# Kernel optimization log

Measured on AMD Instinct MI355X. Metric: run time of the kernel, lower is better.

## Reference

```python
import jax, jax.numpy as jnp
import numpy as np
from math import sqrt

N = 8192
INPUT_SIZE = 256
D_MODEL = 256


def setup_inputs() -> dict:
    key = jax.random.key(0)
    k1, k2, k3, k4 = jax.random.split(key, 4)
    x = jax.random.normal(k1, (N, INPUT_SIZE), dtype=jnp.float32)
    adj = jax.random.randint(k2, (N, N), 0, 2, dtype=jnp.int32)
    # torch nn.Linear(input_size, d_model): weight [d_model, input_size], bias [d_model]
    bound = 1.0 / sqrt(INPUT_SIZE)
    Vw = jax.random.uniform(k3, (D_MODEL, INPUT_SIZE), dtype=jnp.float32, minval=-bound, maxval=bound)
    Vb = jax.random.uniform(k4, (D_MODEL,), dtype=jnp.float32, minval=-bound, maxval=bound)
    return {"x": x, "adj": adj, "Vw": Vw, "Vb": Vb}


def reference(x, adj, Vw, Vb):
    # value = V(x)
    value = x @ Vw.T + Vb                                  # [N, d_model]
    # scores = x x^T / sqrt(d_model), masked where adj == 0
    scores = (x @ x.T) * (1.0 / sqrt(D_MODEL))             # [N, N]
    scores = jnp.where(adj == 0, jnp.float32(-1e9), scores)
    p_attn = jax.nn.softmax(scores, axis=-1)               # [N, N]
    Vs = p_attn @ value                                    # [N, d_model]
    return (Vs, p_attn)
```

## Files before the change

### kernel.cpp

```cpp
#include <hip/hip_runtime.h>
#include <hip/hip_bf16.h>


#define NN 8192
#define DD 256

typedef __attribute__((ext_vector_type(8))) short bf16x8;
typedef __attribute__((ext_vector_type(4))) float f32x4;

__device__ __forceinline__ unsigned short f2bf(float f) {
  unsigned u = __builtin_bit_cast(unsigned, f);
  u += 0x7fffu + ((u >> 16) & 1u);
  return (unsigned short)(u >> 16);
}
__device__ __forceinline__ float bf2f(unsigned short h) {
  unsigned u = ((unsigned)h) << 16;
  return __builtin_bit_cast(float, u);
}
__device__ __forceinline__ unsigned pack2(float a, float b) {
  return (unsigned)f2bf(a) | ((unsigned)f2bf(b) << 16);
}

__global__ void k_prep_x(const float* __restrict__ x, unsigned short* __restrict__ xb) {
  int t = blockIdx.x * 256 + threadIdx.x;
  const float4* s = reinterpret_cast<const float4*>(x) + (size_t)t * 2;
  float4 f0 = s[0], f1 = s[1];
  uint4 o;
  o.x = pack2(f0.x, f0.y); o.y = pack2(f0.z, f0.w);
  o.z = pack2(f1.x, f1.y); o.w = pack2(f1.z, f1.w);
  reinterpret_cast<uint4*>(xb)[t] = o;
}

__global__ __launch_bounds__(256) void k_value(
    const float* __restrict__ Vw, const float* __restrict__ Vb,
    const unsigned short* __restrict__ xb, unsigned short* __restrict__ vT) {
  __shared__ unsigned short lB[64 * 256];
  int mb = blockIdx.x >> 2, nb = blockIdx.x & 3;
  int tid = threadIdx.x, lane = tid & 63, w = tid >> 6;
  int mw = w >> 1, nw = w & 1;
  {
    int n_l = tid >> 2, q = tid & 3;
#pragma unroll
    for (int o = 0; o < 8; ++o) {
      int k0 = q * 64 + o * 8;
      const float4* src = reinterpret_cast<const float4*>(Vw + (nb * 64 + n_l) * DD + k0);
      float4 g0 = src[0], g1 = src[1];
      uint4 pk;
      pk.x = pack2(g0.x, g0.y); pk.y = pack2(g0.z, g0.w);
      pk.z = pack2(g1.x, g1.y); pk.w = pack2(g1.z, g1.w);
      *reinterpret_cast<uint4*>(reinterpret_cast<char*>(lB) + n_l * 512 + ((k0 * 2) ^ ((n_l & 7) << 4))) = pk;
    }
  }
  bf16x8 aR[2][8];
#pragma unroll
  for (int mf = 0; mf < 2; ++mf) {
    int rg = mb * 64 + mw * 32 + mf * 16 + (lane & 15);
    const char* base = reinterpret_cast<const char*>(xb + (size_t)rg * DD);
#pragma unroll
    for (int ks = 0; ks < 8; ++ks)
      aR[mf][ks] = *reinterpret_cast<const bf16x8*>(base + ks * 64 + ((lane >> 4) * 16));
  }
  __syncthreads();
  f32x4 acc[2][2] = {};
#pragma unroll
  for (int ks = 0; ks < 8; ++ks) {
    int kb = ks * 64 + ((lane >> 4) * 16);
#pragma unroll
    for (int nf = 0; nf < 2; ++nf) {
      int n = nw * 32 + nf * 16 + (lane & 15);
      bf16x8 b = *reinterpret_cast<const bf16x8*>(reinterpret_cast<const char*>(lB) + n * 512 + (kb ^ ((n & 7) << 4)));
#pragma unroll
      for (int mf = 0; mf < 2; ++mf)
        acc[mf][nf] = __builtin_amdgcn_mfma_f32_16x16x32_bf16(aR[mf][ks], b, acc[mf][nf], 0, 0, 0);
    }
  }
#pragma unroll
  for (int nf = 0; nf < 2; ++nf) {
    int n_g = nb * 64 + nw * 32 + nf * 16 + (lane & 15);
    float vb = Vb[n_g];
#pragma unroll
    for (int mf = 0; mf < 2; ++mf) {
      int m_g = mb * 64 + mw * 32 + mf * 16 + ((lane >> 4) << 2);
      ushort4 h;
      h.x = f2bf(acc[mf][nf][0] + vb);
      h.y = f2bf(acc[mf][nf][1] + vb);
      h.z = f2bf(acc[mf][nf][2] + vb);
      h.w = f2bf(acc[mf][nf][3] + vb);
      *reinterpret_cast<ushort4*>(vT + (size_t)n_g * NN + m_g) = h;
    }
  }
}

__global__ __launch_bounds__(256) void k_pass1(
    const unsigned short* __restrict__ xb, const int* __restrict__ adj,
    unsigned short* __restrict__ ews, float* __restrict__ lpart) {
  __shared__ char smem[65536];
  int rb = blockIdx.x >> 6, cb = blockIdx.x & 63;
  int tid = threadIdx.x, lane = tid & 63, w = tid >> 6;
  int mw = w >> 1, wc = w & 1;
#pragma unroll
  for (int c = 0; c < 16; ++c) {
    int id = c * 256 + tid;
    int col = id >> 5, oct = id & 31;
    uint4 v = *reinterpret_cast<const uint4*>(xb + (size_t)(cb * 128 + col) * DD + oct * 8);
    *reinterpret_cast<uint4*>(smem + col * 512 + ((oct * 16) ^ ((col & 7) << 4))) = v;
  }
  bf16x8 aR[2][8];
#pragma unroll
  for (int mf = 0; mf < 2; ++mf) {
    int rg = rb * 64 + mw * 32 + mf * 16 + (lane & 15);
    const char* base = reinterpret_cast<const char*>(xb + (size_t)rg * DD);
#pragma unroll
    for (int ks = 0; ks < 8; ++ks)
      aR[mf][ks] = *reinterpret_cast<const bf16x8*>(base + ks * 64 + ((lane >> 4) * 16));
  }
  __syncthreads();
  int r0 = rb * 64 + mw * 32 + ((lane >> 4) << 2);
  int c0 = cb * 128 + wc * 64 + (lane & 15);
  int aj[2][4][4];
#pragma unroll
  for (int mf = 0; mf < 2; ++mf)
#pragma unroll
    for (int nf = 0; nf < 4; ++nf)
#pragma unroll
      for (int i = 0; i < 4; ++i)
        aj[mf][nf][i] = adj[(size_t)(r0 + mf * 16 + i) * NN + (c0 + nf * 16)];
  f32x4 acc[2][4] = {};
#pragma unroll
  for (int ks = 0; ks < 8; ++ks) {
    int kb = ks * 64 + ((lane >> 4) * 16);
#pragma unroll
    for (int nf = 0; nf < 4; ++nf) {
      int cc = wc * 64 + nf * 16 + (lane & 15);
      bf16x8 b = *reinterpret_cast<const bf16x8*>(smem + cc * 512 + (kb ^ ((cc & 7) << 4)));
#pragma unroll
      for (int mf = 0; mf < 2; ++mf)
        acc[mf][nf] = __builtin_amdgcn_mfma_f32_16x16x32_bf16(aR[mf][ks], b, acc[mf][nf], 0, 0, 0);
    }
  }
#pragma unroll
  for (int mf = 0; mf < 2; ++mf)
#pragma unroll
    for (int nf = 0; nf < 4; ++nf)
#pragma unroll
      for (int i = 0; i < 4; ++i) {
        float e = aj[mf][nf][i] ? __expf(acc[mf][nf][i] * 0.0625f) : 0.f;
        unsigned short h = f2bf(e);
        ews[(size_t)(r0 + mf * 16 + i) * NN + (c0 + nf * 16)] = h;
        acc[mf][nf][i] = bf2f(h);
      }
  __syncthreads();
  float* ls = reinterpret_cast<float*>(smem);
#pragma unroll
  for (int mf = 0; mf < 2; ++mf)
#pragma unroll
    for (int i = 0; i < 4; ++i) {
      float r = acc[mf][0][i] + acc[mf][1][i] + acc[mf][2][i] + acc[mf][3][i];
      r += __shfl_xor(r, 1); r += __shfl_xor(r, 2);
      r += __shfl_xor(r, 4); r += __shfl_xor(r, 8);
      if ((lane & 15) == 0)
        ls[wc * 64 + mw * 32 + mf * 16 + ((lane >> 4) << 2) + i] = r;
    }
  __syncthreads();
  if (tid < 64)
    lpart[(size_t)cb * NN + rb * 64 + tid] = ls[tid] + ls[64 + tid];
}

__global__ void k_reduce_l(const float* __restrict__ lpart, float* __restrict__ rl) {
  int i = blockIdx.x * 256 + threadIdx.x;
  float s = 0.f;
  for (int c = 0; c < 64; ++c) s += lpart[(size_t)c * NN + i];
  rl[i] = s > 0.f ? 1.f / s : 0.f;
}

__global__ __launch_bounds__(512) void k_pass2(
    const unsigned short* __restrict__ ews, const unsigned short* __restrict__ vT,
    const float* __restrict__ rl, float* __restrict__ pout, float* __restrict__ vsp) {
  __shared__ unsigned short lA[32 * 64];
  __shared__ unsigned short lB[256 * 64];
  int rb = blockIdx.x >> 1, ch = blockIdx.x & 1;
  int tid = threadIdx.x, lane = tid & 63, w = tid >> 6;
  int wr = w >> 2, wc = w & 3;
  int r0 = rb * 32, j0 = ch * 4096;
  int arow = tid >> 3, aoct = tid & 7;
  float rlA = 0.f;
  if (tid < 256) rlA = rl[r0 + arow];
  f32x4 acc[4] = {};
  for (int kt = 0; kt < 64; ++kt) {
    int jb = j0 + kt * 64;
    uint4 vA;
    if (tid < 256) vA = *reinterpret_cast<const uint4*>(ews + (size_t)(r0 + arow) * NN + jb + aoct * 8);
    uint4 vB[4];
#pragma unroll
    for (int q = 0; q < 4; ++q) {
      int id = q * 512 + tid, n = id >> 3, o = id & 7;
      vB[q] = *reinterpret_cast<const uint4*>(vT + (size_t)n * NN + jb + o * 8);
    }
    if (tid < 256) {
      const unsigned short* hh = reinterpret_cast<const unsigned short*>(&vA);
      float4 p0, p1;
      p0.x = bf2f(hh[0]) * rlA; p0.y = bf2f(hh[1]) * rlA;
      p0.z = bf2f(hh[2]) * rlA; p0.w = bf2f(hh[3]) * rlA;
      p1.x = bf2f(hh[4]) * rlA; p1.y = bf2f(hh[5]) * rlA;
      p1.z = bf2f(hh[6]) * rlA; p1.w = bf2f(hh[7]) * rlA;
      float4* pd = reinterpret_cast<float4*>(pout + (size_t)(r0 + arow) * NN + jb + aoct * 8);
      pd[0] = p0; pd[1] = p1;
      *reinterpret_cast<uint4*>(reinterpret_cast<char*>(lA) + arow * 128 + ((aoct * 16) ^ ((arow & 7) << 4))) = vA;
    }
#pragma unroll
    for (int q = 0; q < 4; ++q) {
      int id = q * 512 + tid, n = id >> 3, o = id & 7;
      *reinterpret_cast<uint4*>(reinterpret_cast<char*>(lB) + n * 128 + ((o * 16) ^ ((n & 7) << 4))) = vB[q];
    }
    __syncthreads();
#pragma unroll
    for (int ksp = 0; ksp < 2; ++ksp) {
      int kb = ksp * 64 + ((lane >> 4) * 16);
      int r = wr * 16 + (lane & 15);
      bf16x8 a = *reinterpret_cast<const bf16x8*>(reinterpret_cast<const char*>(lA) + r * 128 + (kb ^ ((r & 7) << 4)));
#pragma unroll
      for (int nf = 0; nf < 4; ++nf) {
        int n = wc * 64 + nf * 16 + (lane & 15);
        bf16x8 b = *reinterpret_cast<const bf16x8*>(reinterpret_cast<const char*>(lB) + n * 128 + (kb ^ ((n & 7) << 4)));
        acc[nf] = __builtin_amdgcn_mfma_f32_16x16x32_bf16(a, b, acc[nf], 0, 0, 0);
      }
    }
    __syncthreads();
  }
  float rli[4];
  int rbase = r0 + wr * 16 + ((lane >> 4) << 2);
#pragma unroll
  for (int i = 0; i < 4; ++i) rli[i] = rl[rbase + i];
#pragma unroll
  for (int nf = 0; nf < 4; ++nf) {
    int n = wc * 64 + nf * 16 + (lane & 15);
#pragma unroll
    for (int i = 0; i < 4; ++i)
      vsp[(size_t)(ch * NN + rbase + i) * DD + n] = acc[nf][i] * rli[i];
  }
}

__global__ void k_reduce_vs(const float* __restrict__ vsp, float* __restrict__ vout) {
  int t = blockIdx.x * 256 + threadIdx.x;
  float4 a = *reinterpret_cast<const float4*>(vsp + (size_t)t * 4);
  float4 b = *reinterpret_cast<const float4*>(vsp + (size_t)NN * DD + (size_t)t * 4);
  float4 r;
  r.x = a.x + b.x; r.y = a.y + b.y; r.z = a.z + b.z; r.w = a.w + b.w;
  *reinterpret_cast<float4*>(vout + (size_t)t * 4) = r;
}

extern "C" void kernel_launch(void* const* d_in, const int* in_sizes, int n_in,
                              void* d_out, int out_size, void* d_ws, size_t ws_size,
                              hipStream_t stream) {
  const float* x   = (const float*)d_in[0];
  const int*   adj = (const int*)d_in[1];
  const float* Vw  = (const float*)d_in[2];
  const float* Vb  = (const float*)d_in[3];
  float* out   = (float*)d_out;
  float* vs_out = out;
  float* p_out  = out + (size_t)NN * DD;
  char* ws = (char*)d_ws;
  unsigned short* xb  = (unsigned short*)(ws);
  unsigned short* vT  = (unsigned short*)(ws + ((size_t)4  << 20));
  float* lpart        = (float*)(ws + ((size_t)8  << 20));
  float* rl           = (float*)(ws + ((size_t)10 << 20));
  float* vsp          = (float*)(ws + ((size_t)11 << 20));
  unsigned short* ews = (unsigned short*)(ws + ((size_t)27 << 20));

  k_prep_x<<<dim3(1024), dim3(256), 0, stream>>>(x, xb);
  k_value<<<dim3(512), dim3(256), 0, stream>>>(Vw, Vb, xb, vT);
  k_pass1<<<dim3(8192), dim3(256), 0, stream>>>(xb, adj, ews, lpart);
  k_reduce_l<<<dim3(32), dim3(256), 0, stream>>>(lpart, rl);
  k_pass2<<<dim3(512), dim3(512), 0, stream>>>(ews, vT, rl, p_out, vsp);
  k_reduce_vs<<<dim3(2048), dim3(256), 0, stream>>>(vsp, vs_out);
}
```

Before: 365.5 us.

## Restructure pass2 with 128-row tiles, register A fragments, and double-buffered B

After: 498.3 us. +36.3%, slower.

```diff
diff --git a/kernel.cpp b/kernel.cpp
--- a/kernel.cpp
+++ b/kernel.cpp
@@ -6,6 +6,7 @@
 #define DD 256
 
 typedef __attribute__((ext_vector_type(8))) short bf16x8;
+typedef __attribute__((ext_vector_type(8))) unsigned short u16x8;
 typedef __attribute__((ext_vector_type(4))) float f32x4;
 
 __device__ __forceinline__ unsigned short f2bf(float f) {
@@ -175,78 +176,100 @@
 
 __global__ __launch_bounds__(512) void k_pass2(
     const unsigned short* __restrict__ ews, const unsigned short* __restrict__ vT,
-    const float* __restrict__ rl, float* __restrict__ pout, float* __restrict__ vsp) {
-  __shared__ unsigned short lA[32 * 64];
-  __shared__ unsigned short lB[256 * 64];
-  int rb = blockIdx.x >> 1, ch = blockIdx.x & 1;
+    const float* __restrict__ rl, float* __restrict__ pout, unsigned short* __restrict__ vspb) {
+  __shared__ char lB[2][32768];
+  int rb = blockIdx.x >> 2, ch = blockIdx.x & 3;
   int tid = threadIdx.x, lane = tid & 63, w = tid >> 6;
-  int wr = w >> 2, wc = w & 3;
-  int r0 = rb * 32, j0 = ch * 4096;
-  int arow = tid >> 3, aoct = tid & 7;
-  float rlA = 0.f;
-  if (tid < 256) rlA = rl[r0 + arow];
-  f32x4 acc[4] = {};
-  for (int kt = 0; kt < 64; ++kt) {
-    int jb = j0 + kt * 64;
-    uint4 vA;
-    if (tid < 256) vA = *reinterpret_cast<const uint4*>(ews + (size_t)(r0 + arow) * NN + jb + aoct * 8);
-    uint4 vB[4];
-#pragma unroll
-    for (int q = 0; q < 4; ++q) {
-      int id = q * 512 + tid, n = id >> 3, o = id & 7;
-      vB[q] = *reinterpret_cast<const uint4*>(vT + (size_t)n * NN + jb + o * 8);
-    }
-    if (tid < 256) {
-      const unsigned short* hh = reinterpret_cast<const unsigned short*>(&vA);
-      float4 p0, p1;
-      p0.x = bf2f(hh[0]) * rlA; p0.y = bf2f(hh[1]) * rlA;
-      p0.z = bf2f(hh[2]) * rlA; p0.w = bf2f(hh[3]) * rlA;
-      p1.x = bf2f(hh[4]) * rlA; p1.y = bf2f(hh[5]) * rlA;
-      p1.z = bf2f(hh[6]) * rlA; p1.w = bf2f(hh[7]) * rlA;
-      float4* pd = reinterpret_cast<float4*>(pout + (size_t)(r0 + arow) * NN + jb + aoct * 8);
-      pd[0] = p0; pd[1] = p1;
-      *reinterpret_cast<uint4*>(reinterpret_cast<char*>(lA) + arow * 128 + ((aoct * 16) ^ ((arow & 7) << 4))) = vA;
-    }
-#pragma unroll
-    for (int q = 0; q < 4; ++q) {
-      int id = q * 512 + tid, n = id >> 3, o = id & 7;
-      *reinterpret_cast<uint4*>(reinterpret_cast<char*>(lB) + n * 128 + ((o * 16) ^ ((n & 7) << 4))) = vB[q];
-    }
-    __syncthreads();
+  int kq = lane >> 4;
+  int row = rb * 128 + w * 16 + (lane & 15);
+  size_t erow = (size_t)row * NN;
+  int k0 = ch * 2048;
+  float rlv = rl[row];
+
+#define LOADB(G, KT)                                                                   \
+  _Pragma("unroll") for (int q = 0; q < 4; ++q) {                                      \
+    int seg = q * 512 + tid, n_ = seg >> 3, c_ = seg & 7;                              \
+    (G)[q] = *reinterpret_cast<const uint4*>(vT + (size_t)n_ * NN + k0 + (KT) * 64 + c_ * 8); \
+  }
+#define DSWRITE(G, BB)                                                                 \
+  _Pragma("unroll") for (int q = 0; q < 4; ++q) {                                      \
+    int seg = q * 512 + tid, n_ = seg >> 3, c_ = seg & 7;                              \
+    *reinterpret_cast<uint4*>(&lB[BB][n_ * 128 + ((c_ * 16) ^ ((n_ & 7) << 4))]) = (G)[q]; \
+  }
+#define LOADA(A0, A1, KT)                                                              \
+  (A0) = *reinterpret_cast<const bf16x8*>(ews + erow + k0 + (KT) * 64 + kq * 8);       \
+  (A1) = *reinterpret_cast<const bf16x8*>(ews + erow + k0 + (KT) * 64 + 32 + kq * 8);
+
+  uint4 gB[4];
+  bf16x8 aC0, aC1, aN0, aN1;
+  LOADB(gB, 0);
+  LOADA(aC0, aC1, 0);
+  DSWRITE(gB, 0);
+  __syncthreads();
+
+  f32x4 acc[16] = {};
+  for (int kt = 0; kt < 32; ++kt) {
+    bool has = kt < 31;
+    if (has) {
+      LOADB(gB, kt + 1);
+      LOADA(aN0, aN1, kt + 1);
+    }
+    const char* bufc = lB[kt & 1];
 #pragma unroll
     for (int ksp = 0; ksp < 2; ++ksp) {
-      int kb = ksp * 64 + ((lane >> 4) * 16);
-      int r = wr * 16 + (lane & 15);
-      bf16x8 a = *reinterpret_cast<const bf16x8*>(reinterpret_cast<const char*>(lA) + r * 128 + (kb ^ ((r & 7) << 4)));
-#pragma unroll
-      for (int nf = 0; nf < 4; ++nf) {
-        int n = wc * 64 + nf * 16 + (lane & 15);
-        bf16x8 b = *reinterpret_cast<const bf16x8*>(reinterpret_cast<const char*>(lB) + n * 128 + (kb ^ ((n & 7) << 4)));
+      bf16x8 a = ksp ? aC1 : aC0;
+#pragma unroll
+      for (int nf = 0; nf < 16; ++nf) {
+        int n = nf * 16 + (lane & 15);
+        bf16x8 b = *reinterpret_cast<const bf16x8*>(bufc + n * 128 + ((ksp * 64 + kq * 16) ^ ((n & 7) << 4)));
         acc[nf] = __builtin_amdgcn_mfma_f32_16x16x32_bf16(a, b, acc[nf], 0, 0, 0);
       }
     }
+#pragma unroll
+    for (int ksp = 0; ksp < 2; ++ksp) {
+      bf16x8 a = ksp ? aC1 : aC0;
+      float4 p0, p1;
+      p0.x = bf2f((unsigned short)a[0]) * rlv; p0.y = bf2f((unsigned short)a[1]) * rlv;
+      p0.z = bf2f((unsigned short)a[2]) * rlv; p0.w = bf2f((unsigned short)a[3]) * rlv;
+      p1.x = bf2f((unsigned short)a[4]) * rlv; p1.y = bf2f((unsigned short)a[5]) * rlv;
+      p1.z = bf2f((unsigned short)a[6]) * rlv; p1.w = bf2f((unsigned short)a[7]) * rlv;
+      float4* pd = reinterpret_cast<float4*>(pout + erow + k0 + kt * 64 + ksp * 32 + kq * 8);
+      pd[0] = p0; pd[1] = p1;
+    }
+    if (has) DSWRITE(gB, (kt + 1) & 1);
     __syncthreads();
-  }
-  float rli[4];
-  int rbase = r0 + wr * 16 + ((lane >> 4) << 2);
-#pragma unroll
-  for (int i = 0; i < 4; ++i) rli[i] = rl[rbase + i];
-#pragma unroll
-  for (int nf = 0; nf < 4; ++nf) {
-    int n = wc * 64 + nf * 16 + (lane & 15);
-#pragma unroll
-    for (int i = 0; i < 4; ++i)
-      vsp[(size_t)(ch * NN + rbase + i) * DD + n] = acc[nf][i] * rli[i];
-  }
-}
-
-__global__ void k_reduce_vs(const float* __restrict__ vsp, float* __restrict__ vout) {
+    aC0 = aN0; aC1 = aN1;
+  }
+
+  int rowo = rb * 128 + w * 16 + kq * 4;
+#pragma unroll
+  for (int i = 0; i < 4; ++i) {
+    float rli = rl[rowo + i];
+#pragma unroll
+    for (int nf = 0; nf < 16; ++nf) {
+      int n = nf * 16 + (lane & 15);
+      vspb[((size_t)ch * NN + rowo + i) * DD + n] = f2bf(acc[nf][i] * rli);
+    }
+  }
+#undef LOADB
+#undef DSWRITE
+#undef LOADA
+}
+
+__global__ void k_reduce_vs(const unsigned short* __restrict__ vspb, float* __restrict__ vout) {
   int t = blockIdx.x * 256 + threadIdx.x;
-  float4 a = *reinterpret_cast<const float4*>(vsp + (size_t)t * 4);
-  float4 b = *reinterpret_cast<const float4*>(vsp + (size_t)NN * DD + (size_t)t * 4);
-  float4 r;
-  r.x = a.x + b.x; r.y = a.y + b.y; r.z = a.z + b.z; r.w = a.w + b.w;
-  *reinterpret_cast<float4*>(vout + (size_t)t * 4) = r;
+  float s[8] = {};
+#pragma unroll
+  for (int c = 0; c < 4; ++c) {
+    u16x8 v = *reinterpret_cast<const u16x8*>(vspb + (size_t)c * NN * DD + (size_t)t * 8);
+#pragma unroll
+    for (int j = 0; j < 8; ++j) s[j] += bf2f(v[j]);
+  }
+  float4 o0, o1;
+  o0.x = s[0]; o0.y = s[1]; o0.z = s[2]; o0.w = s[3];
+  o1.x = s[4]; o1.y = s[5]; o1.z = s[6]; o1.w = s[7];
+  float4* d = reinterpret_cast<float4*>(vout + (size_t)t * 8);
+  d[0] = o0; d[1] = o1;
 }
 
 extern "C" void kernel_launch(void* const* d_in, const int* in_sizes, int n_in,
@@ -260,17 +283,17 @@
   float* vs_out = out;
   float* p_out  = out + (size_t)NN * DD;
   char* ws = (char*)d_ws;
-  unsigned short* xb  = (unsigned short*)(ws);
-  unsigned short* vT  = (unsigned short*)(ws + ((size_t)4  << 20));
-  float* lpart        = (float*)(ws + ((size_t)8  << 20));
-  float* rl           = (float*)(ws + ((size_t)10 << 20));
-  float* vsp          = (float*)(ws + ((size_t)11 << 20));
-  unsigned short* ews = (unsigned short*)(ws + ((size_t)27 << 20));
+  unsigned short* xb   = (unsigned short*)(ws);
+  unsigned short* vT   = (unsigned short*)(ws + ((size_t)4  << 20));
+  float* lpart         = (float*)(ws + ((size_t)8  << 20));
+  float* rl            = (float*)(ws + ((size_t)10 << 20));
+  unsigned short* vspb = (unsigned short*)(ws + ((size_t)11 << 20));
+  unsigned short* ews  = (unsigned short*)(ws + ((size_t)27 << 20));
 
   k_prep_x<<<dim3(1024), dim3(256), 0, stream>>>(x, xb);
   k_value<<<dim3(512), dim3(256), 0, stream>>>(Vw, Vb, xb, vT);
   k_pass1<<<dim3(8192), dim3(256), 0, stream>>>(xb, adj, ews, lpart);
   k_reduce_l<<<dim3(32), dim3(256), 0, stream>>>(lpart, rl);
-  k_pass2<<<dim3(512), dim3(512), 0, stream>>>(ews, vT, rl, p_out, vsp);
-  k_reduce_vs<<<dim3(2048), dim3(256), 0, stream>>>(vsp, vs_out);
-}
+  k_pass2<<<dim3(256), dim3(512), 0, stream>>>(ews, vT, rl, p_out, vspb);
+  k_reduce_vs<<<dim3(1024), dim3(256), 0, stream>>>(vspb, vs_out);
+}
```
